# Kernel optimization log

Measured on AMD Instinct MI355X. Metric: run time of the kernel, lower is better.

Reference implementation:

```python
import jax, jax.numpy as jnp
import numpy as np

N, P, IN, HID, HEADS, OUT, E = 8192, 3, 256, 64, 8, 64, 262144
HD = HEADS * HID


def _gat(h, fc, al, ar, bias, src, dst):
    # DGL GATConv forward (no dropout), returns (elu(out) [N,H,D], attention [E,H])
    feat = (h @ fc).reshape(N, HEADS, HID)          # [N,H,D]
    el = (feat * al).sum(-1)                        # [N,H]
    er = (feat * ar).sum(-1)                        # [N,H]
    e = jax.nn.leaky_relu(el[src] + er[dst], negative_slope=0.2)  # [E,H]
    emax = jax.ops.segment_max(e, dst, num_segments=N)            # [N,H]
    ee = jnp.exp(e - emax[dst])
    denom = jax.ops.segment_sum(ee, dst, num_segments=N)          # [N,H]
    a = ee / denom[dst]                                           # edge softmax over dst
    rst = jax.ops.segment_sum(a[:, :, None] * feat[src], dst, num_segments=N)  # [N,H,D]
    out = jax.nn.elu(rst + bias)
    return out, a


def setup_inputs():
    key = jax.random.key(0)
    ks = jax.random.split(key, 12)
    s = 0.05
    return {
        "h": jax.random.normal(ks[0], (N, IN), jnp.float32),
        "edge_src": jax.random.randint(ks[1], (P, E), 0, N, jnp.int32),
        "edge_dst": jax.random.randint(ks[2], (P, E), 0, N, jnp.int32),
        "gat_fc": jax.random.normal(ks[3], (P, IN, HD), jnp.float32) * s,
        "attn_l": jax.random.normal(ks[4], (P, HEADS, HID), jnp.float32) * s,
        "attn_r": jax.random.normal(ks[5], (P, HEADS, HID), jnp.float32) * s,
        "gat_bias": jnp.zeros((P, HEADS, HID), jnp.float32),
        "sa_w1": jax.random.normal(ks[6], (HD, 128), jnp.float32) * s,
        "sa_b1": jnp.zeros((128,), jnp.float32),
        "sa_w2": jax.random.normal(ks[7], (128, 1), jnp.float32) * s,
        "pred_w": jax.random.normal(ks[8], (HD, OUT), jnp.float32) * s,
        "pred_b": jnp.zeros((OUT,), jnp.float32),
    }


def reference(h, edge_src, edge_dst, gat_fc, attn_l, attn_r, gat_bias,
              sa_w1, sa_b1, sa_w2, pred_w, pred_b):
    zp_list, alpha_list = [], []
    for p in range(P):
        z_p, a_p = _gat(h, gat_fc[p], attn_l[p], attn_r[p], gat_bias[p],
                        edge_src[p], edge_dst[p])
        zp_list.append(z_p.reshape(N, HD))          # flatten(start_dim=1)
        alpha_list.append(a_p.mean(axis=1))         # [E], mean over heads
    zp = jnp.stack(zp_list, axis=1)                 # [N,P,HD]

    # Semantic attention
    w = (zp @ sa_w1 + sa_b1) @ sa_w2                # [N,P,1]
    w = jax.nn.leaky_relu(w, negative_slope=0.01).mean(axis=0)  # [P,1]
    beta = jax.nn.softmax(w, axis=0)                # [P,1]

    # Dense adjacency accumulation of edge attention weights
    atten = jnp.zeros((N, N), jnp.float32)
    for p in range(P):
        vals = alpha_list[p] * beta[p, 0]
        atten = atten.at[edge_src[p], edge_dst[p]].add(vals)

    z = (beta[None, :, :] * zp).sum(axis=1)         # [N,HD]
    out = z @ pred_w + pred_b                       # [N,OUT]
    return out, atten
```

## Files before the change

### kernel.cpp

```cpp
#include <hip/hip_runtime.h>
#include <math.h>

#define NN    8192
#define PP    3
#define INF_  256
#define HID_  64
#define HEADS 8
#define OUTF  64
#define NE    262144
#define HD    512
#define DEGCAP 128

typedef __attribute__((ext_vector_type(8))) short short8;
typedef __attribute__((ext_vector_type(4))) float f32x4;

__device__ __forceinline__ unsigned short f2bf(float f) {
    unsigned u = __float_as_uint(f);
    unsigned r = u + 0x7fffu + ((u >> 16) & 1u);
    return (unsigned short)(r >> 16);
}
__device__ __forceinline__ float bf2f_lo(unsigned v) { return __uint_as_float(v << 16); }
__device__ __forceinline__ float bf2f_hi(unsigned v) { return __uint_as_float(v & 0xffff0000u); }

__device__ __forceinline__ void beta_reg(const float* __restrict__ wsum,
                                         float& rb0, float& rb1, float& rb2) {
    int lane = threadIdx.x & 63;
    float s0 = wsum[lane], s1 = wsum[64 + lane], s2 = wsum[128 + lane];
#pragma unroll
    for (int off = 32; off > 0; off >>= 1) {
        s0 += __shfl_down(s0, off);
        s1 += __shfl_down(s1, off);
        s2 += __shfl_down(s2, off);
    }
    float t0 = __shfl(s0, 0), t1 = __shfl(s1, 0), t2 = __shfl(s2, 0);
    float w0 = t0 / (float)NN, w1 = t1 / (float)NN, w2 = t2 / (float)NN;
    float m  = fmaxf(w0, fmaxf(w1, w2));
    float e0 = expf(w0 - m), e1 = expf(w1 - m), e2 = expf(w2 - m);
    float ss = e0 + e1 + e2;
    rb0 = e0 / ss; rb1 = e1 / ss; rb2 = e2 / ss;
}

__global__ __launch_bounds__(256) void cast_count(
        const float* __restrict__ h, const float* __restrict__ fc,
        const int* __restrict__ esrc, const int* __restrict__ edst,
        unsigned short* __restrict__ hb, unsigned short* __restrict__ fcT,
        int* __restrict__ counts ) {
    int b = blockIdx.x, t = threadIdx.x;
    if (b < 2048) {
        int i = b * 256 + t;
        float4 v = *(const float4*)(h + (size_t)i * 4);
        ushort4 o = { f2bf(v.x), f2bf(v.y), f2bf(v.z), f2bf(v.w) };
        *(ushort4*)(hb + (size_t)i * 4) = o;
    } else if (b < 2048 + 1536) {
        int i = (b - 2048) * 256 + t;
        if (i < PP * INF_ * HD) {
            int p = i / (INF_ * HD);
            int rem = i - p * INF_ * HD;
            int k = rem / HD;
            int n = rem - k * HD;
            fcT[(size_t)p * HD * INF_ + (size_t)n * INF_ + k] = f2bf(fc[i]);
        }
    } else {
        int i = (b - 3584) * 256 + t;
        int4 s4 = ((const int4*)esrc)[i];
        int4 d4 = ((const int4*)edst)[i];
        int p = i >> 16;
        atomicAdd(&counts[p * NN + d4.x], 1);
        atomicAdd(&counts[p * NN + d4.y], 1);
        atomicAdd(&counts[p * NN + d4.z], 1);
        atomicAdd(&counts[p * NN + d4.w], 1);
        atomicAdd(&counts[3 * NN + s4.x], 1);
        atomicAdd(&counts[3 * NN + s4.y], 1);
        atomicAdd(&counts[3 * NN + s4.z], 1);
        atomicAdd(&counts[3 * NN + s4.w], 1);
    }
}

__global__ __launch_bounds__(1024) void scan_vw(
        const int* __restrict__ counts, int* __restrict__ offsets,
        int* __restrict__ cursor, const float* __restrict__ w1,
        const float* __restrict__ b1, const float* __restrict__ w2,
        float* __restrict__ v ) {
    int t = threadIdx.x;
    if (blockIdx.x == 4) {
        if (t < HD) {
            float s = 0.f;
            for (int k = 0; k < 128; ++k) s += w1[t * 128 + k] * w2[k];
            v[t] = s;
        } else if (t == HD) {
            float c = 0.f;
            for (int k = 0; k < 128; ++k) c += b1[k] * w2[k];
            v[HD] = c;
        }
        return;
    }
    __shared__ int sh[1024];
    int seg = blockIdx.x;
    const int* cnt = counts + seg * NN;
    int* offs = offsets + seg * (NN + 1);
    int* cur  = cursor + seg * NN;
    int loc[8];
    int s = 0;
#pragma unroll
    for (int i = 0; i < 8; ++i) { loc[i] = cnt[t * 8 + i]; s += loc[i]; }
    sh[t] = s;
    __syncthreads();
    for (int off = 1; off < 1024; off <<= 1) {
        int vv = (t >= off) ? sh[t - off] : 0;
        __syncthreads();
        sh[t] += vv;
        __syncthreads();
    }
    int run = sh[t] - s;
#pragma unroll
    for (int i = 0; i < 8; ++i) {
        offs[t * 8 + i] = run;
        cur[t * 8 + i]  = run;
        run += loc[i];
    }
    if (t == 1023) offs[NN] = run;
}

#define LDK 72
__global__ __launch_bounds__(256) void scatter_gemm(
        const int* __restrict__ esrc, const int* __restrict__ edst,
        int* __restrict__ cursor, int* __restrict__ ssrc_sorted,
        int2* __restrict__ spair,
        const unsigned short* __restrict__ hb,
        const unsigned short* __restrict__ fcT,
        const float* __restrict__ al_all,
        const float* __restrict__ ar_all,
        unsigned short* __restrict__ featb,
        float* __restrict__ el,
        float* __restrict__ er) {
    __shared__ unsigned short As[64 * LDK];
    __shared__ unsigned short Bs[64 * LDK];
    int tid = threadIdx.x;
    if (blockIdx.x < 3072) {
        int i = blockIdx.x * 256 + tid;
        int p = i >> 18;
        int s = esrc[i], d = edst[i];
        int pos = atomicAdd(&cursor[p * NN + d], 1);
        ssrc_sorted[(size_t)p * NE + pos] = s;
        int pos2 = atomicAdd(&cursor[3 * NN + s], 1);
        int2 pr; pr.x = p * NE + pos; pr.y = d;
        spair[pos2] = pr;
        return;
    }
    int g  = blockIdx.x - 3072;
    int p  = g >> 10;
    int n0 = (g & 7) * 64;
    int m0 = ((g >> 3) & 127) * 64;
    const unsigned short* Bt = fcT + (size_t)p * HD * INF_;
    unsigned short* C = featb + (size_t)p * NN * HD;
    int wv   = tid >> 6, lane = tid & 63;
    int row  = tid >> 2, kc = (tid & 3) * 8;
    int l16  = lane & 15, quad = lane >> 4;
    int mw   = wv * 16;
    f32x4 acc[4] = {{0.f,0.f,0.f,0.f},{0.f,0.f,0.f,0.f},
                    {0.f,0.f,0.f,0.f},{0.f,0.f,0.f,0.f}};
    for (int k0 = 0; k0 < INF_; k0 += 64) {
        const unsigned short* ha = &hb[(size_t)(m0 + row) * INF_ + k0 + kc];
        const unsigned short* ba = &Bt[(size_t)(n0 + row) * INF_ + k0 + kc];
        *(short8*)&As[row * LDK + kc]      = *(const short8*)ha;
        *(short8*)&As[row * LDK + kc + 32] = *(const short8*)(ha + 32);
        *(short8*)&Bs[row * LDK + kc]      = *(const short8*)ba;
        *(short8*)&Bs[row * LDK + kc + 32] = *(const short8*)(ba + 32);
        __syncthreads();
        short8 af0 = *(short8*)&As[(mw + l16) * LDK + quad * 8];
        short8 af1 = *(short8*)&As[(mw + l16) * LDK + 32 + quad * 8];
#pragma unroll
        for (int nt = 0; nt < 4; ++nt) {
            short8 bf0 = *(short8*)&Bs[(nt * 16 + l16) * LDK + quad * 8];
            acc[nt] = __builtin_amdgcn_mfma_f32_16x16x32_bf16(af0, bf0, acc[nt], 0, 0, 0);
            short8 bf1 = *(short8*)&Bs[(nt * 16 + l16) * LDK + 32 + quad * 8];
            acc[nt] = __builtin_amdgcn_mfma_f32_16x16x32_bf16(af1, bf1, acc[nt], 0, 0, 0);
        }
        __syncthreads();
    }
#pragma unroll
    for (int nt = 0; nt < 4; ++nt) {
#pragma unroll
        for (int r = 0; r < 4; ++r) {
            C[(size_t)(m0 + mw + quad * 4 + r) * HD + n0 + nt * 16 + l16] =
                f2bf(acc[nt][r]);
        }
    }
    int hidx = n0 >> 6;
    float alv[4], arv[4];
#pragma unroll
    for (int nt = 0; nt < 4; ++nt) {
        alv[nt] = al_all[p * HD + n0 + nt * 16 + l16];
        arv[nt] = ar_all[p * HD + n0 + nt * 16 + l16];
    }
    float* elp = el + (size_t)p * NN * HEADS;
    float* erp = er + (size_t)p * NN * HEADS;
#pragma unroll
    for (int r = 0; r < 4; ++r) {
        float pe = acc[0][r] * alv[0] + acc[1][r] * alv[1] +
                   acc[2][r] * alv[2] + acc[3][r] * alv[3];
        float pr = acc[0][r] * arv[0] + acc[1][r] * arv[1] +
                   acc[2][r] * arv[2] + acc[3][r] * arv[3];
#pragma unroll
        for (int m = 1; m < 16; m <<= 1) {
            pe += __shfl_xor(pe, m);
            pr += __shfl_xor(pr, m);
        }
        if (l16 == 0) {
            int node = m0 + mw + quad * 4 + r;
            elp[node * HEADS + hidx] = pe;
            erp[node * HEADS + hidx] = pr;
        }
    }
}

__global__ __launch_bounds__(256) void fused_attn_rst(
        const int* __restrict__ ssrc_sorted, const int* __restrict__ offsets_all,
        const float* __restrict__ el, const float* __restrict__ er,
        const unsigned short* __restrict__ featb,
        const float* __restrict__ bias_all, const float* __restrict__ v,
        float* __restrict__ alpha_all ,
        unsigned short* __restrict__ zpb,
        float* __restrict__ wsum ) {
    __shared__ float sh_e[4][DEGCAP * 8];
    __shared__ int   sh_src[4][DEGCAP];
    int wv = threadIdx.x >> 6, lane = threadIdx.x & 63;
    int gid = blockIdx.x * 4 + wv;
    int n = gid & (NN - 1);
    int p = gid >> 13;
    const int* srcrow  = ssrc_sorted + (size_t)p * NE;
    const int* offs    = offsets_all + p * (NN + 1);
    const float* elp   = el + (size_t)p * NN * HEADS;
    const float* erp   = er + (size_t)p * NN * HEADS;
    const unsigned short* feat = featb + (size_t)p * NN * HD;
    int start = offs[n];
    int deg = offs[n + 1] - start;
    if (deg > DEGCAP) deg = DEGCAP;

    float4 r0 = *(const float4*)(erp + n * 8);
    float4 r1 = *(const float4*)(erp + n * 8 + 4);
    for (int t = lane; t < deg; t += 64) {
        int s = srcrow[start + t];
        sh_src[wv][t] = s;
        float4 l0 = *(const float4*)(elp + s * 8);
        float4 l1 = *(const float4*)(elp + s * 8 + 4);
        float sc[8] = {l0.x + r0.x, l0.y + r0.y, l0.z + r0.z, l0.w + r0.w,
                       l1.x + r1.x, l1.y + r1.y, l1.z + r1.z, l1.w + r1.w};
#pragma unroll
        for (int hh = 0; hh < 8; ++hh) {
            float x = sc[hh];
            sh_e[wv][t * 8 + hh] = x > 0.f ? x : 0.2f * x;
        }
    }
    __syncthreads();

    int h = lane >> 3;
    {
        int j = lane & 7;
        float m = -INFINITY;
        for (int t = j; t < deg; t += 8) m = fmaxf(m, sh_e[wv][t * 8 + h]);
#pragma unroll
        for (int off = 4; off; off >>= 1) m = fmaxf(m, __shfl_xor(m, off));
        float ssum = 0.f;
        for (int t = j; t < deg; t += 8) {
            float ee = __expf(sh_e[wv][t * 8 + h] - m);
            sh_e[wv][t * 8 + h] = ee;
            ssum += ee;
        }
#pragma unroll
        for (int off = 4; off; off >>= 1) ssum += __shfl_xor(ssum, off);
        float inv = 1.f / ssum;
        for (int t = j; t < deg; t += 8) sh_e[wv][t * 8 + h] *= inv;
    }
    __syncthreads();

    for (int t = lane; t < deg; t += 64) {
        float s = 0.f;
#pragma unroll
        for (int hh = 0; hh < 8; ++hh) s += sh_e[wv][t * 8 + hh];
        alpha_all[(size_t)p * NE + start + t] = s * 0.125f;
    }

    int c = lane * 8;
    float acc[8] = {0.f, 0.f, 0.f, 0.f, 0.f, 0.f, 0.f, 0.f};
#define FMA8(F, KI) { \
        float a_ = sh_e[wv][(KI) * 8 + h]; \
        acc[0] += a_ * bf2f_lo((F).x); acc[1] += a_ * bf2f_hi((F).x); \
        acc[2] += a_ * bf2f_lo((F).y); acc[3] += a_ * bf2f_hi((F).y); \
        acc[4] += a_ * bf2f_lo((F).z); acc[5] += a_ * bf2f_hi((F).z); \
        acc[6] += a_ * bf2f_lo((F).w); acc[7] += a_ * bf2f_hi((F).w); }
    int k = 0;
    for (; k + 4 <= deg; k += 4) {
        int s0 = sh_src[wv][k],     s1 = sh_src[wv][k + 1];
        int s2 = sh_src[wv][k + 2], s3 = sh_src[wv][k + 3];
        uint4 f0 = *(const uint4*)&feat[(size_t)s0 * HD + c];
        uint4 f1 = *(const uint4*)&feat[(size_t)s1 * HD + c];
        uint4 f2 = *(const uint4*)&feat[(size_t)s2 * HD + c];
        uint4 f3 = *(const uint4*)&feat[(size_t)s3 * HD + c];
        FMA8(f0, k); FMA8(f1, k + 1); FMA8(f2, k + 2); FMA8(f3, k + 3);
    }
    for (; k < deg; ++k) {
        int s = sh_src[wv][k];
        uint4 f = *(const uint4*)&feat[(size_t)s * HD + c];
        FMA8(f, k);
    }
#undef FMA8
    const float* bias = bias_all + p * HD;
    float4 b0 = *(const float4*)(bias + c);
    float4 b1 = *(const float4*)(bias + c + 4);
    float z[8];
    z[0] = acc[0] + b0.x; z[1] = acc[1] + b0.y; z[2] = acc[2] + b0.z; z[3] = acc[3] + b0.w;
    z[4] = acc[4] + b1.x; z[5] = acc[5] + b1.y; z[6] = acc[6] + b1.z; z[7] = acc[7] + b1.w;
#pragma unroll
    for (int i = 0; i < 8; ++i) z[i] = z[i] > 0.f ? z[i] : expm1f(z[i]);
    uint4 zo;
    zo.x = (unsigned)f2bf(z[0]) | ((unsigned)f2bf(z[1]) << 16);
    zo.y = (unsigned)f2bf(z[2]) | ((unsigned)f2bf(z[3]) << 16);
    zo.z = (unsigned)f2bf(z[4]) | ((unsigned)f2bf(z[5]) << 16);
    zo.w = (unsigned)f2bf(z[6]) | ((unsigned)f2bf(z[7]) << 16);
    *(uint4*)&zpb[(size_t)n * (PP * HD) + p * HD + c] = zo;

    float4 v0 = *(const float4*)(v + c);
    float4 v1 = *(const float4*)(v + c + 4);
    float part = z[0] * v0.x + z[1] * v0.y + z[2] * v0.z + z[3] * v0.w +
                 z[4] * v1.x + z[5] * v1.y + z[6] * v1.z + z[7] * v1.w;
#pragma unroll
    for (int off = 32; off > 0; off >>= 1) part += __shfl_down(part, off);
    if (lane == 0) {
        float w = part + v[HD];
        w = w > 0.f ? w : 0.01f * w;
        atomicAdd(&wsum[p * 64 + (n & 63)], w);
    }
}

#define K5R 16
__global__ __launch_bounds__(256) void final_atten(
        const unsigned short* __restrict__ zpb, const float* __restrict__ wsum,
        const float* __restrict__ pw, const float* __restrict__ pb,
        const int2* __restrict__ spair, const int* __restrict__ soffs,
        const float* __restrict__ alpha,
        float* __restrict__ out, float* __restrict__ atten) {
    __shared__ float buf[NN];
    float b0, b1, b2;
    beta_reg(wsum, b0, b1, b2);
    int tid = threadIdx.x;
    if (blockIdx.x < NN) {
        int srow = blockIdx.x;
        f32x4 zero = {0.f, 0.f, 0.f, 0.f};
        for (int j = tid; j < NN / 4; j += 256) ((f32x4*)buf)[j] = zero;
        __syncthreads();
        int s0 = soffs[srow], s1 = soffs[srow + 1];
        for (int k = s0 + tid; k < s1; k += 256) {
            int2 pr = spair[k];
            int pp = pr.x >> 18;
            float bsel = pp == 0 ? b0 : (pp == 1 ? b1 : b2);
            atomicAdd(&buf[pr.y], alpha[pr.x] * bsel);
        }
        __syncthreads();
        float* orow = atten + (size_t)srow * NN;
        for (int j = tid * 4; j < NN; j += 1024) {
            f32x4 v = *(f32x4*)(buf + j);
            __builtin_nontemporal_store(v, (f32x4*)(orow + j));
        }
    } else {
        int n0 = (blockIdx.x - NN) * K5R;
        float* zt = buf;
        int c = tid * 2;
#pragma unroll
        for (int r = 0; r < K5R; ++r) {
            const unsigned short* zr = zpb + (size_t)(n0 + r) * (PP * HD);
            unsigned u0 = *(const unsigned*)(zr + c);
            unsigned u1 = *(const unsigned*)(zr + HD + c);
            unsigned u2 = *(const unsigned*)(zr + 2 * HD + c);
            zt[r * HD + c]     = b0 * bf2f_lo(u0) + b1 * bf2f_lo(u1) + b2 * bf2f_lo(u2);
            zt[r * HD + c + 1] = b0 * bf2f_hi(u0) + b1 * bf2f_hi(u1) + b2 * bf2f_hi(u2);
        }
        __syncthreads();
        int o = tid & 63, rg = tid >> 6;
        float a0 = 0.f, a1 = 0.f, a2 = 0.f, a3 = 0.f;
        for (int j = 0; j < HD; ++j) {
            float pwj = pw[j * 64 + o];
            a0 += zt[(rg * 4 + 0) * HD + j] * pwj;
            a1 += zt[(rg * 4 + 1) * HD + j] * pwj;
            a2 += zt[(rg * 4 + 2) * HD + j] * pwj;
            a3 += zt[(rg * 4 + 3) * HD + j] * pwj;
        }
        float bo = pb[o];
        out[(size_t)(n0 + rg * 4 + 0) * 64 + o] = a0 + bo;
        out[(size_t)(n0 + rg * 4 + 1) * 64 + o] = a1 + bo;
        out[(size_t)(n0 + rg * 4 + 2) * 64 + o] = a2 + bo;
        out[(size_t)(n0 + rg * 4 + 3) * 64 + o] = a3 + bo;
    }
}

extern "C" void kernel_launch(void* const* d_in, const int* in_sizes, int n_in,
                              void* d_out, int out_size, void* d_ws, size_t ws_size,
                              hipStream_t stream) {
    const float* h    = (const float*)d_in[0];
    const int*   esrc = (const int*)d_in[1];
    const int*   edst = (const int*)d_in[2];
    const float* fc   = (const float*)d_in[3];
    const float* al   = (const float*)d_in[4];
    const float* ar   = (const float*)d_in[5];
    const float* bias = (const float*)d_in[6];
    const float* w1   = (const float*)d_in[7];
    const float* b1   = (const float*)d_in[8];
    const float* w2   = (const float*)d_in[9];
    const float* pw   = (const float*)d_in[10];
    const float* pb   = (const float*)d_in[11];
    float* out   = (float*)d_out;
    float* atten = out + (size_t)NN * OUTF;

    char* ws = (char*)d_ws;
    size_t off = 0;
    auto alloc = [&](size_t bytes) {
        void* p = ws + off;
        off = (off + bytes + 255) & ~(size_t)255;
        return p;
    };
    unsigned short* zpb   = (unsigned short*)alloc(sizeof(short) * (size_t)NN * PP * HD);
    unsigned short* featb = (unsigned short*)alloc(sizeof(short) * (size_t)PP * NN * HD);
    unsigned short* hb  = (unsigned short*)alloc(sizeof(short) * (size_t)NN * INF_);
    unsigned short* fcT = (unsigned short*)alloc(sizeof(short) * (size_t)PP * HD * INF_);
    float*  el      = (float*)alloc(sizeof(float) * PP * NN * HEADS);
    float*  er      = (float*)alloc(sizeof(float) * PP * NN * HEADS);
    float*  alpha   = (float*)alloc(sizeof(float) * (size_t)PP * NE);
    int*    counts  = (int*)alloc(sizeof(int) * 4 * NN);
    float*  wsum    = (float*)alloc(sizeof(float) * 3 * 64);
    int*    offsets = (int*)alloc(sizeof(int) * 4 * (NN + 1));
    int*    cursor  = (int*)alloc(sizeof(int) * 4 * NN);
    int*    ssrc_sorted = (int*)alloc(sizeof(int) * (size_t)PP * NE);
    int2*   spair   = (int2*)alloc(sizeof(int2) * (size_t)PP * NE);
    float*  vbuf    = (float*)alloc(sizeof(float) * (HD + 1));

    (void)hipMemsetAsync(counts, 0, sizeof(int) * 4 * NN + 1024, stream);

    cast_count<<<2048 + 1536 + 768, 256, 0, stream>>>(
        h, fc, esrc, edst, hb, fcT, counts);

    scan_vw<<<5, 1024, 0, stream>>>(counts, offsets, cursor, w1, b1, w2, vbuf);

    scatter_gemm<<<6144, 256, 0, stream>>>(
        esrc, edst, cursor, ssrc_sorted, spair,
        hb, fcT, al, ar, featb, el, er);

    fused_attn_rst<<<NN * PP / 4, 256, 0, stream>>>(
        ssrc_sorted, offsets, el, er, featb, bias, vbuf, alpha, zpb, wsum);

    final_atten<<<NN + NN / K5R, 256, 0, stream>>>(
        zpb, wsum, pw, pb, spair, offsets + 3 * (NN + 1), alpha, out, atten);
}
```

Before: 657.3 us.

## Drop source-sorted CSR; zero atten early and scatter with global atomics

Removes the second (source-keyed) CSR and its spair buffer. The dense 8192x8192 atten matrix is now zero-filled with nontemporal stores inside the first kernel, and final_atten does per-destination global atomicAdds into atten[s*N+n] instead of building each row in shared memory. Edges are sub-bucketed by (dst, src>>10) so each destination's sources are roughly sorted, which improves locality of the scattered atomics. The cost is 786K global float atomics to a 256MB buffer, plus a larger count/scan array (64 entries per scan thread instead of 8).

After: 693.6 us. 1.06x slower.

```diff
diff --git a/kernel.cpp b/kernel.cpp
--- a/kernel.cpp
+++ b/kernel.cpp
@@ -10,6 +10,9 @@
 #define NE    262144
 #define HD    512
 #define DEGCAP 128
+#define NB    8
+#define DOFF  (NB * NN)
+#define POFF  (NB * NN + 1)
 
 typedef __attribute__((ext_vector_type(8))) short short8;
 typedef __attribute__((ext_vector_type(4))) float f32x4;
@@ -44,7 +47,8 @@
         const float* __restrict__ h, const float* __restrict__ fc,
         const int* __restrict__ esrc, const int* __restrict__ edst,
         unsigned short* __restrict__ hb, unsigned short* __restrict__ fcT,
-        int* __restrict__ counts ) {
+        int* __restrict__ counts ,
+        float* __restrict__ atten) {
     int b = blockIdx.x, t = threadIdx.x;
     if (b < 2048) {
         int i = b * 256 + t;
@@ -60,19 +64,23 @@
             int n = rem - k * HD;
             fcT[(size_t)p * HD * INF_ + (size_t)n * INF_ + k] = f2bf(fc[i]);
         }
-    } else {
+    } else if (b < 2048 + 1536 + 768) {
         int i = (b - 3584) * 256 + t;
         int4 s4 = ((const int4*)esrc)[i];
         int4 d4 = ((const int4*)edst)[i];
         int p = i >> 16;
-        atomicAdd(&counts[p * NN + d4.x], 1);
-        atomicAdd(&counts[p * NN + d4.y], 1);
-        atomicAdd(&counts[p * NN + d4.z], 1);
-        atomicAdd(&counts[p * NN + d4.w], 1);
-        atomicAdd(&counts[3 * NN + s4.x], 1);
-        atomicAdd(&counts[3 * NN + s4.y], 1);
-        atomicAdd(&counts[3 * NN + s4.z], 1);
-        atomicAdd(&counts[3 * NN + s4.w], 1);
+        int base = p * DOFF;
+        atomicAdd(&counts[base + (d4.x << 3) + (s4.x >> 10)], 1);
+        atomicAdd(&counts[base + (d4.y << 3) + (s4.y >> 10)], 1);
+        atomicAdd(&counts[base + (d4.z << 3) + (s4.z >> 10)], 1);
+        atomicAdd(&counts[base + (d4.w << 3) + (s4.w >> 10)], 1);
+    } else {
+        f32x4* a4 = (f32x4*)atten;
+        int idx0 = (b - 4352) * 256 + t;
+        f32x4 zero = {0.f, 0.f, 0.f, 0.f};
+#pragma unroll 4
+        for (int it = 0; it < 64; ++it)
+            __builtin_nontemporal_store(zero, &a4[(size_t)it * 262144 + idx0]);
     }
 }
 
@@ -82,7 +90,7 @@
         const float* __restrict__ b1, const float* __restrict__ w2,
         float* __restrict__ v ) {
     int t = threadIdx.x;
-    if (blockIdx.x == 4) {
+    if (blockIdx.x == 3) {
         if (t < HD) {
             float s = 0.f;
             for (int k = 0; k < 128; ++k) s += w1[t * 128 + k] * w2[k];
@@ -96,13 +104,11 @@
     }
     __shared__ int sh[1024];
     int seg = blockIdx.x;
-    const int* cnt = counts + seg * NN;
-    int* offs = offsets + seg * (NN + 1);
-    int* cur  = cursor + seg * NN;
-    int loc[8];
+    const int* cnt = counts + seg * DOFF;
+    int* offs = offsets + seg * POFF;
+    int* cur  = cursor + seg * DOFF;
     int s = 0;
-#pragma unroll
-    for (int i = 0; i < 8; ++i) { loc[i] = cnt[t * 8 + i]; s += loc[i]; }
+    for (int i = 0; i < 64; ++i) s += cnt[t * 64 + i];
     sh[t] = s;
     __syncthreads();
     for (int off = 1; off < 1024; off <<= 1) {
@@ -112,20 +118,19 @@
         __syncthreads();
     }
     int run = sh[t] - s;
-#pragma unroll
-    for (int i = 0; i < 8; ++i) {
-        offs[t * 8 + i] = run;
-        cur[t * 8 + i]  = run;
-        run += loc[i];
-    }
-    if (t == 1023) offs[NN] = run;
+    for (int i = 0; i < 64; ++i) {
+        int c = cnt[t * 64 + i];
+        offs[t * 64 + i] = run;
+        cur[t * 64 + i]  = run;
+        run += c;
+    }
+    if (t == 1023) offs[DOFF] = run;
 }
 
 #define LDK 72
 __global__ __launch_bounds__(256) void scatter_gemm(
         const int* __restrict__ esrc, const int* __restrict__ edst,
         int* __restrict__ cursor, int* __restrict__ ssrc_sorted,
-        int2* __restrict__ spair,
         const unsigned short* __restrict__ hb,
         const unsigned short* __restrict__ fcT,
         const float* __restrict__ al_all,
@@ -140,11 +145,8 @@
         int i = blockIdx.x * 256 + tid;
         int p = i >> 18;
         int s = esrc[i], d = edst[i];
-        int pos = atomicAdd(&cursor[p * NN + d], 1);
+        int pos = atomicAdd(&cursor[p * DOFF + (d << 3) + (s >> 10)], 1);
         ssrc_sorted[(size_t)p * NE + pos] = s;
-        int pos2 = atomicAdd(&cursor[3 * NN + s], 1);
-        int2 pr; pr.x = p * NE + pos; pr.y = d;
-        spair[pos2] = pr;
         return;
     }
     int g  = blockIdx.x - 3072;
@@ -229,12 +231,12 @@
     int n = gid & (NN - 1);
     int p = gid >> 13;
     const int* srcrow  = ssrc_sorted + (size_t)p * NE;
-    const int* offs    = offsets_all + p * (NN + 1);
+    const int* offs    = offsets_all + p * POFF;
     const float* elp   = el + (size_t)p * NN * HEADS;
     const float* erp   = er + (size_t)p * NN * HEADS;
     const unsigned short* feat = featb + (size_t)p * NN * HD;
-    int start = offs[n];
-    int deg = offs[n + 1] - start;
+    int start = offs[n * NB];
+    int deg = offs[n * NB + NB] - start;
     if (deg > DEGCAP) deg = DEGCAP;
 
     float4 r0 = *(const float4*)(erp + n * 8);
@@ -337,34 +339,31 @@
 __global__ __launch_bounds__(256) void final_atten(
         const unsigned short* __restrict__ zpb, const float* __restrict__ wsum,
         const float* __restrict__ pw, const float* __restrict__ pb,
-        const int2* __restrict__ spair, const int* __restrict__ soffs,
+        const int* __restrict__ ssrc_sorted, const int* __restrict__ offsets_all,
         const float* __restrict__ alpha,
         float* __restrict__ out, float* __restrict__ atten) {
-    __shared__ float buf[NN];
     float b0, b1, b2;
     beta_reg(wsum, b0, b1, b2);
     int tid = threadIdx.x;
-    if (blockIdx.x < NN) {
-        int srow = blockIdx.x;
-        f32x4 zero = {0.f, 0.f, 0.f, 0.f};
-        for (int j = tid; j < NN / 4; j += 256) ((f32x4*)buf)[j] = zero;
-        __syncthreads();
-        int s0 = soffs[srow], s1 = soffs[srow + 1];
-        for (int k = s0 + tid; k < s1; k += 256) {
-            int2 pr = spair[k];
-            int pp = pr.x >> 18;
-            float bsel = pp == 0 ? b0 : (pp == 1 ? b1 : b2);
-            atomicAdd(&buf[pr.y], alpha[pr.x] * bsel);
-        }
-        __syncthreads();
-        float* orow = atten + (size_t)srow * NN;
-        for (int j = tid * 4; j < NN; j += 1024) {
-            f32x4 v = *(f32x4*)(buf + j);
-            __builtin_nontemporal_store(v, (f32x4*)(orow + j));
+    if (blockIdx.x < NN * PP / 4) {
+        int wv = tid >> 6, lane = tid & 63;
+        int gid = blockIdx.x * 4 + wv;
+        int n = gid & (NN - 1);
+        int p = gid >> 13;
+        float bsel = p == 0 ? b0 : (p == 1 ? b1 : b2);
+        const int* offs = offsets_all + p * POFF;
+        int start = offs[n * NB];
+        int deg = offs[n * NB + NB] - start;
+        if (deg > DEGCAP) deg = DEGCAP;
+        const int* srcrow = ssrc_sorted + (size_t)p * NE + start;
+        const float* arow = alpha + (size_t)p * NE + start;
+        for (int t = lane; t < deg; t += 64) {
+            int s = srcrow[t];
+            atomicAdd(&atten[(size_t)s * NN + n], arow[t] * bsel);
         }
     } else {
-        int n0 = (blockIdx.x - NN) * K5R;
-        float* zt = buf;
+        __shared__ float zt[K5R * HD];
+        int n0 = (blockIdx.x - NN * PP / 4) * K5R;
         int c = tid * 2;
 #pragma unroll
         for (int r = 0; r < K5R; ++r) {
@@ -425,28 +424,27 @@
     float*  el      = (float*)alloc(sizeof(float) * PP * NN * HEADS);
     float*  er      = (float*)alloc(sizeof(float) * PP * NN * HEADS);
     float*  alpha   = (float*)alloc(sizeof(float) * (size_t)PP * NE);
-    int*    counts  = (int*)alloc(sizeof(int) * 4 * NN);
+    int*    counts  = (int*)alloc(sizeof(int) * 3 * DOFF);
     float*  wsum    = (float*)alloc(sizeof(float) * 3 * 64);
-    int*    offsets = (int*)alloc(sizeof(int) * 4 * (NN + 1));
-    int*    cursor  = (int*)alloc(sizeof(int) * 4 * NN);
+    int*    offsets = (int*)alloc(sizeof(int) * 3 * POFF);
+    int*    cursor  = (int*)alloc(sizeof(int) * 3 * DOFF);
     int*    ssrc_sorted = (int*)alloc(sizeof(int) * (size_t)PP * NE);
-    int2*   spair   = (int2*)alloc(sizeof(int2) * (size_t)PP * NE);
     float*  vbuf    = (float*)alloc(sizeof(float) * (HD + 1));
 
-    (void)hipMemsetAsync(counts, 0, sizeof(int) * 4 * NN + 1024, stream);
-
-    cast_count<<<2048 + 1536 + 768, 256, 0, stream>>>(
-        h, fc, esrc, edst, hb, fcT, counts);
-
-    scan_vw<<<5, 1024, 0, stream>>>(counts, offsets, cursor, w1, b1, w2, vbuf);
+    (void)hipMemsetAsync(counts, 0, sizeof(int) * 3 * DOFF + 1024, stream);
+
+    cast_count<<<2048 + 1536 + 768 + 1024, 256, 0, stream>>>(
+        h, fc, esrc, edst, hb, fcT, counts, atten);
+
+    scan_vw<<<4, 1024, 0, stream>>>(counts, offsets, cursor, w1, b1, w2, vbuf);
 
     scatter_gemm<<<6144, 256, 0, stream>>>(
-        esrc, edst, cursor, ssrc_sorted, spair,
+        esrc, edst, cursor, ssrc_sorted,
         hb, fcT, al, ar, featb, el, er);
 
     fused_attn_rst<<<NN * PP / 4, 256, 0, stream>>>(
         ssrc_sorted, offsets, el, er, featb, bias, vbuf, alpha, zpb, wsum);
 
-    final_atten<<<NN + NN / K5R, 256, 0, stream>>>(
-        zpb, wsum, pw, pb, spair, offsets + 3 * (NN + 1), alpha, out, atten);
-}
+    final_atten<<<NN * PP / 4 + NN / K5R, 256, 0, stream>>>(
+        zpb, wsum, pw, pb, ssrc_sorted, offsets, alpha, out, atten);
+}
```
